# Kernel optimization log

Hardware: AMD Instinct MI355X
Metric: run time of the kernel (lower is better)

The kernel has to match this reference:

```python
import jax, jax.numpy as jnp
import numpy as np

N_GRAPHS = 8
NODES_PER_G = 1024
EDGES_PER_G = 2048
N = N_GRAPHS * NODES_PER_G          # 8192 nodes
E = N_GRAPHS * EDGES_PER_G          # 16384 edges
IN_DIM, EDGE_DIM, HID, OUT_DIM, T = 10, 9, 64, 3, 5
EPS = 1e-6


def _lin(key, fan_in, fan_out):
    kw, kb = jax.random.split(key)
    s = 1.0 / np.sqrt(fan_in)
    return (jax.random.uniform(kw, (fan_in, fan_out), jnp.float32, -s, s),
            jax.random.uniform(kb, (fan_out,), jnp.float32, -s, s))


def setup_inputs() -> dict:
    key = jax.random.key(0)
    ks = jax.random.split(key, 32)
    x = jax.random.normal(ks[0], (N, IN_DIM), jnp.float32)
    edge_attr = jax.random.normal(ks[1], (E, EDGE_DIM), jnp.float32)
    # edges stay within their own graph (block structure)
    src_l = jax.random.randint(ks[2], (E,), 0, NODES_PER_G)
    dst_l = jax.random.randint(ks[3], (E,), 0, NODES_PER_G)
    off = jnp.repeat(jnp.arange(N_GRAPHS, dtype=jnp.int64) * NODES_PER_G, EDGES_PER_G)
    edge_index = jnp.stack([src_l.astype(jnp.int64) + off, dst_l.astype(jnp.int64) + off])
    batch = jnp.repeat(jnp.arange(N_GRAPHS, dtype=jnp.int64), NODES_PER_G)

    lift_w1, lift_b1 = _lin(ks[4], IN_DIM, HID)
    lift_w2, lift_b2 = _lin(ks[5], HID, HID)
    proj_w1, proj_b1 = _lin(ks[6], HID, HID)
    proj_w2, proj_b2 = _lin(ks[7], HID, OUT_DIM)

    def stackp(fn, base):
        ws, bs = zip(*[fn(ks[base + t]) for t in range(T)])
        return jnp.stack(ws), jnp.stack(bs)

    root_w, root_b = stackp(lambda k: _lin(k, HID, HID), 8)
    k_w1, k_b1 = stackp(lambda k: _lin(k, EDGE_DIM, HID), 13)
    k_w2, k_b2 = stackp(lambda k: _lin(k, HID, HID), 18)
    k_w3, k_b3 = stackp(lambda k: _lin(k, HID, HID * HID), 23)

    return dict(x=x, edge_attr=edge_attr,
                lift_w1=lift_w1, lift_b1=lift_b1, lift_w2=lift_w2, lift_b2=lift_b2,
                root_w=root_w, root_b=root_b,
                k_w1=k_w1, k_b1=k_b1, k_w2=k_w2, k_b2=k_b2, k_w3=k_w3, k_b3=k_b3,
                proj_w1=proj_w1, proj_b1=proj_b1, proj_w2=proj_w2, proj_b2=proj_b2,
                edge_index=edge_index, batch=batch)


def reference(x, edge_attr, lift_w1, lift_b1, lift_w2, lift_b2,
              root_w, root_b, k_w1, k_b1, k_w2, k_b2, k_w3, k_b3,
              proj_w1, proj_b1, proj_w2, proj_b2, edge_index, batch):
    src, dst = edge_index[0], edge_index[1]

    # --- per-graph edge_attr standardization (scatter mean/std over each graph's edges) ---
    eb = batch[src]                                           # graph id per edge [E]
    ones_e = jnp.ones((E,), jnp.float32)
    cnt = jax.ops.segment_sum(ones_e, eb, num_segments=N_GRAPHS)          # [G]
    mean = jax.ops.segment_sum(edge_attr, eb, num_segments=N_GRAPHS) / cnt[:, None]
    msq = jax.ops.segment_sum(edge_attr * edge_attr, eb, num_segments=N_GRAPHS) / cnt[:, None]
    std = jnp.sqrt(jnp.clip(msq - mean * mean, 0.0))
    ea = (edge_attr - mean[eb]) / (std[eb] + EPS)             # [E, edge_dim]

    # --- lift MLP ---
    v = jax.nn.relu(x @ lift_w1 + lift_b1) @ lift_w2 + lift_b2  # [N, HID]

    # --- T kernel layers: v' = relu(W_root v + mean_{j->i} K(e_ij) v_j) ---
    deg = jnp.clip(jax.ops.segment_sum(ones_e, dst, num_segments=N), 1.0)  # [N]
    for t in range(T):
        h = jax.nn.relu(ea @ k_w1[t] + k_b1[t])
        h = jax.nn.relu(h @ k_w2[t] + k_b2[t])
        ker = (h @ k_w3[t] + k_b3[t]).reshape(E, HID, HID)    # per-edge 64x64 kernel
        msg = jnp.einsum('eij,ej->ei', ker, v[src])           # [E, HID]
        aggr = jax.ops.segment_sum(msg, dst, num_segments=N) / deg[:, None]
        v = jax.nn.relu(v @ root_w[t] + root_b[t] + aggr)
        # dropout (p=0.1) is identity in eval mode

    # --- project MLP ---
    return jax.nn.relu(v @ proj_w1 + proj_b1) @ proj_w2 + proj_b2  # [N, OUT_DIM]
```

## Files before the change

kernel.cpp:

```cpp
#include <hip/hip_runtime.h>

#define N_GRAPHS    8
#define EDGES_PER_G 2048
#define NN          8192
#define EE          16384
#define IN_DIM      10
#define EDGE_DIM    9
#define HID         64
#define OUT_DIM     3
#define TT          5
#define EPSN        1e-6f

typedef float f32x4 __attribute__((ext_vector_type(4)));
typedef short bf16x8s __attribute__((ext_vector_type(8)));

union BF8 { __bf16 h[8]; bf16x8s v; };

__device__ inline void gl_lds16(const unsigned short* g, unsigned short* l) {
  __builtin_amdgcn_global_load_lds(
      (const __attribute__((address_space(1))) unsigned int*)g,
      (__attribute__((address_space(3))) unsigned int*)l, 16, 0, 0);
}

__device__ inline void edgemlp16(int e0, int tid,
    const float* __restrict__ ear, const float* __restrict__ meanb,
    const float* __restrict__ invstd,
    const float* __restrict__ w1, const float* __restrict__ b1,
    const float* __restrict__ w2, const float* __restrict__ b2,
    float* smem, float* __restrict__ h2T) {
  float (*sh)[68] = (float (*)[68])smem;
  float (*st)[68] = (float (*)[68])(smem + 16 * 68);
  int g = tid >> 6, lane = tid & 63;
  int eb = e0 + g * 4;
  int gg = e0 >> 11;
  const float* mb = meanb + gg * EDGE_DIM;
  const float* is = invstd + gg * EDGE_DIM;
  float xn[4][EDGE_DIM];
#pragma unroll
  for (int k = 0; k < 4; ++k) {
    const float* er = ear + (size_t)(eb + k) * EDGE_DIM;
#pragma unroll
    for (int d = 0; d < EDGE_DIM; ++d) xn[k][d] = (er[d] - mb[d]) * is[d];
  }
  float a0 = b1[lane], a1 = a0, a2 = a0, a3 = a0;
#pragma unroll
  for (int d = 0; d < EDGE_DIM; ++d) {
    float w = w1[d * HID + lane];
    a0 += xn[0][d] * w; a1 += xn[1][d] * w;
    a2 += xn[2][d] * w; a3 += xn[3][d] * w;
  }
  sh[g * 4 + 0][lane] = fmaxf(a0, 0.f);
  sh[g * 4 + 1][lane] = fmaxf(a1, 0.f);
  sh[g * 4 + 2][lane] = fmaxf(a2, 0.f);
  sh[g * 4 + 3][lane] = fmaxf(a3, 0.f);
  __syncthreads();
  float o0 = b2[lane], o1 = o0, o2 = o0, o3 = o0;
#pragma unroll
  for (int h = 0; h < HID; ++h) {
    float w = w2[h * HID + lane];
    o0 += sh[g * 4 + 0][h] * w; o1 += sh[g * 4 + 1][h] * w;
    o2 += sh[g * 4 + 2][h] * w; o3 += sh[g * 4 + 3][h] * w;
  }
  st[g * 4 + 0][lane] = fmaxf(o0, 0.f);
  st[g * 4 + 1][lane] = fmaxf(o1, 0.f);
  st[g * 4 + 2][lane] = fmaxf(o2, 0.f);
  st[g * 4 + 3][lane] = fmaxf(o3, 0.f);
  __syncthreads();
  for (int i = tid; i < HID * 16; i += 256) {
    int c = i >> 4, eo = i & 15;
    h2T[(size_t)c * EE + e0 + eo] = st[eo][c];
  }
}

__global__ __launch_bounds__(256) void k_stats(
    const float* __restrict__ ear, float* __restrict__ meanb,
    float* __restrict__ invstd, float* __restrict__ degf) {
  __shared__ float sw[4][2 * EDGE_DIM];
  int b = blockIdx.x;
  int g = threadIdx.x >> 6, lane = threadIdx.x & 63;
  if (b < N_GRAPHS) {
    int gg = b;
    float ls[EDGE_DIM], lq[EDGE_DIM];
#pragma unroll
    for (int d = 0; d < EDGE_DIM; ++d) { ls[d] = 0.f; lq[d] = 0.f; }
    for (int e = threadIdx.x; e < EDGES_PER_G; e += blockDim.x) {
      const float* row = ear + (size_t)(gg * EDGES_PER_G + e) * EDGE_DIM;
#pragma unroll
      for (int d = 0; d < EDGE_DIM; ++d) { float xv = row[d]; ls[d] += xv; lq[d] += xv * xv; }
    }
#pragma unroll
    for (int d = 0; d < EDGE_DIM; ++d) {
#pragma unroll
      for (int off = 32; off > 0; off >>= 1) {
        ls[d] += __shfl_down(ls[d], off);
        lq[d] += __shfl_down(lq[d], off);
      }
    }
    if (lane == 0) {
#pragma unroll
      for (int d = 0; d < EDGE_DIM; ++d) {
        sw[g][d] = ls[d];
        sw[g][EDGE_DIM + d] = lq[d];
      }
    }
    __syncthreads();
    if (threadIdx.x < EDGE_DIM) {
      int d = threadIdx.x;
      float s0 = sw[0][d] + sw[1][d] + sw[2][d] + sw[3][d];
      float q0 = sw[0][EDGE_DIM + d] + sw[1][EDGE_DIM + d] +
                 sw[2][EDGE_DIM + d] + sw[3][EDGE_DIM + d];
      float m  = s0 * (1.0f / EDGES_PER_G);
      float mq = q0 * (1.0f / EDGES_PER_G);
      float var = fmaxf(mq - m * m, 0.f);
      meanb[gg * EDGE_DIM + d]  = m;
      invstd[gg * EDGE_DIM + d] = 1.f / (sqrtf(var) + EPSN);
    }
  } else {
    int idx = (b - N_GRAPHS) * 256 + threadIdx.x;
    ((float4*)degf)[idx] = make_float4(0.f, 0.f, 0.f, 0.f);
  }
}

#define PRE_EM0   (EE / 16)
#define PRE_LIFT  (NN / 4)
#define PRE_BPREP 1024
#define PRE_DEG   (EE / 256)
__global__ __launch_bounds__(256) void k_pre(
    const float* __restrict__ x,
    const float* __restrict__ lw1, const float* __restrict__ lb1,
    const float* __restrict__ lw2, const float* __restrict__ lb2,
    float* __restrict__ v,
    const float* __restrict__ kw3, const float* __restrict__ kb3,
    unsigned short* __restrict__ Bbf,
    const int* __restrict__ dst, float* __restrict__ degf,
    const float* __restrict__ ear, const float* __restrict__ meanb,
    const float* __restrict__ invstd,
    const float* __restrict__ w1, const float* __restrict__ b1,
    const float* __restrict__ w2, const float* __restrict__ b2,
    float* __restrict__ h2T0) {
  __shared__ float smem[2 * 16 * 68];
  int b = blockIdx.x;
  int g = threadIdx.x >> 6, lane = threadIdx.x & 63;
  if (b < PRE_EM0) {
    edgemlp16(b * 16, threadIdx.x, ear, meanb, invstd, w1, b1, w2, b2,
              smem, h2T0);
  } else if (b < PRE_EM0 + PRE_LIFT) {
    float (*sh)[HID] = (float (*)[HID])smem;
    int n = (b - PRE_EM0) * 4 + g;
    const float* xr = x + n * IN_DIM;
    float a = lb1[lane];
#pragma unroll
    for (int d = 0; d < IN_DIM; ++d) a += xr[d] * lw1[d * HID + lane];
    sh[g][lane] = fmaxf(a, 0.f);
    __syncthreads();
    float o = lb2[lane];
#pragma unroll
    for (int h = 0; h < HID; ++h) o += sh[g][h] * lw2[h * HID + lane];
    v[n * HID + lane] = o;
  } else if (b < PRE_EM0 + PRE_LIFT + PRE_BPREP) {
    const int total = TT * 65 * 4096;
    for (int i = (b - (PRE_EM0 + PRE_LIFT)) * 256 + (int)threadIdx.x; i < total;
         i += PRE_BPREP * 256) {
      int xx   = i & 4095;
      int call = i >> 12;
      int t = call / 65;
      int c = call - t * 65;
      int sn = xx >> 9;
      int s  = sn >> 2, nt = sn & 3;
      int l9 = xx & 511;
      int ln = l9 >> 3, jj = l9 & 7;
      int nn15 = ln & 15, qq = ln >> 4;
      int x_in = (nt * 16 + nn15) * 64 + s * 32 + qq * 8 + jj;
      float val = (c < 64) ? kw3[(size_t)(t * 64 + c) * 4096 + x_in]
                           : kb3[(size_t)t * 4096 + x_in];
      union { __bf16 h; unsigned short s16; } u;
      u.h = (__bf16)val;
      Bbf[i] = u.s16;
    }
  } else {
    int e = (b - (PRE_EM0 + PRE_LIFT + PRE_BPREP)) * 256 + threadIdx.x;
    atomicAdd(&degf[dst[e]], 1.f);
  }
}

__global__ __launch_bounds__(256) void k_csr1(const float* __restrict__ degf,
    int* __restrict__ rowptr, int* __restrict__ cur) {
  __shared__ int ps[256];
  int tid = threadIdx.x;
  int base = tid * 32;
  int loc[32];
  int s = 0;
#pragma unroll
  for (int k = 0; k < 32; ++k) { loc[k] = s; s += (int)degf[base + k]; }
  ps[tid] = s;
  __syncthreads();
  if (tid == 0) {
    int a = 0;
    for (int i = 0; i < 256; ++i) { int t = ps[i]; ps[i] = a; a += t; }
    rowptr[NN] = a;
  }
  __syncthreads();
  int off = ps[tid];
#pragma unroll
  for (int k = 0; k < 32; ++k) {
    rowptr[base + k] = off + loc[k];
    cur[base + k]    = off + loc[k];
  }
}

__global__ __launch_bounds__(256) void k_csr2(const int* __restrict__ dst,
    int* __restrict__ cur, int* __restrict__ ecsr) {
  int e = blockIdx.x * 256 + threadIdx.x;
  int d = dst[e];
  int pos = atomicAdd(&cur[d], 1);
  ecsr[pos] = e;
}

__global__ __launch_bounds__(256) void k_msg(const float* __restrict__ v,
    const float* __restrict__ h2T_r, const unsigned short* __restrict__ Bt,
    const int* __restrict__ src,
    float* __restrict__ msgbuf, int nEm,
    const float* __restrict__ ear, const float* __restrict__ meanb,
    const float* __restrict__ invstd,
    const float* __restrict__ w1, const float* __restrict__ b1,
    const float* __restrict__ w2, const float* __restrict__ b2,
    float* __restrict__ h2T_w) {
  __shared__ unsigned short bstage[3][4096];
  int b = blockIdx.x;
  if (b < 1024) {
    int kchunk = b & 3;
    int ebb    = (b >> 2) * 64;
    int w    = threadIdx.x >> 6;
    int lane = threadIdx.x & 63;
    int n15  = lane & 15;
    int q    = lane >> 4;
    int ebase = ebb + w * 16;

    bf16x8s ubf[2];
    {
      int e = ebase + n15;
      const float4* vr = (const float4*)(v + (size_t)src[e] * HID);
      int f0 = q * 2;
#pragma unroll
      for (int s = 0; s < 2; ++s) {
        float4 pa = vr[s * 8 + f0], pb = vr[s * 8 + f0 + 1];
        BF8 u;
        u.h[0] = (__bf16)pa.x; u.h[1] = (__bf16)pa.y;
        u.h[2] = (__bf16)pa.z; u.h[3] = (__bf16)pa.w;
        u.h[4] = (__bf16)pb.x; u.h[5] = (__bf16)pb.y;
        u.h[6] = (__bf16)pb.z; u.h[7] = (__bf16)pb.w;
        ubf[s] = u.v;
      }
    }

    f32x4 acc[4];
#pragma unroll
    for (int nt = 0; nt < 4; ++nt) acc[nt] = (f32x4)0.0f;

    int c0 = kchunk * 16;
    const float* hq = h2T_r + (size_t)c0 * EE + ebase + q * 4;
    const int NCC = (kchunk == 3) ? 17 : 16;

    auto stage = [&](int cc) {
      const unsigned short* gt = (cc < 16)
          ? Bt + (size_t)(c0 + cc) * 4096
          : Bt + (size_t)64 * 4096;
      const unsigned short* gsrc = gt + w * 1024 + lane * 8;
      unsigned short* ldst = &bstage[cc % 3][w * 1024];
      gl_lds16(gsrc, ldst);
      gl_lds16(gsrc + 512, ldst + 512);
    };

    stage(0);
    stage(1);

    for (int cc = 0; cc < NCC; ++cc) {
      asm volatile("s_waitcnt vmcnt(2)" ::: "memory");
      __builtin_amdgcn_s_barrier();
      float4 h4;
      if (cc < 16) h4 = *(const float4*)(hq + (size_t)cc * EE);
      __builtin_amdgcn_sched_barrier(0);
      if (cc + 2 < NCC) stage(cc + 2);
      __builtin_amdgcn_sched_barrier(0);

      const unsigned short* Bs = &bstage[cc % 3][lane * 8];
      bf16x8s bfr[2][4];
#pragma unroll
      for (int s = 0; s < 2; ++s)
#pragma unroll
        for (int nt = 0; nt < 4; ++nt)
          bfr[s][nt] = *(const bf16x8s*)(Bs + (s * 4 + nt) * 512);
      if (cc < 16) {
        f32x4 tmp[4];
#pragma unroll
        for (int nt = 0; nt < 4; ++nt) {
          f32x4 t0 = __builtin_amdgcn_mfma_f32_16x16x32_bf16(
              ubf[0], bfr[0][nt], (f32x4)0.0f, 0, 0, 0);
          tmp[nt] = __builtin_amdgcn_mfma_f32_16x16x32_bf16(
              ubf[1], bfr[1][nt], t0, 0, 0, 0);
        }
#pragma unroll
        for (int nt = 0; nt < 4; ++nt) {
          acc[nt][0] += h4.x * tmp[nt][0];
          acc[nt][1] += h4.y * tmp[nt][1];
          acc[nt][2] += h4.z * tmp[nt][2];
          acc[nt][3] += h4.w * tmp[nt][3];
        }
      } else {
#pragma unroll
        for (int s = 0; s < 2; ++s)
#pragma unroll
          for (int nt = 0; nt < 4; ++nt)
            acc[nt] = __builtin_amdgcn_mfma_f32_16x16x32_bf16(
                ubf[s], bfr[s][nt], acc[nt], 0, 0, 0);
      }
    }

    float* mb = msgbuf + (size_t)kchunk * EE * HID;
#pragma unroll
    for (int r = 0; r < 4; ++r) {
      int e = ebase + q * 4 + r;
#pragma unroll
      for (int nt = 0; nt < 4; ++nt)
        mb[(size_t)e * HID + nt * 16 + n15] = acc[nt][r];
    }
  } else if (b < 1024 + nEm) {
    edgemlp16((b - 1024) * 16, threadIdx.x, ear, meanb, invstd,
              w1, b1, w2, b2, (float*)bstage, h2T_w);
  }
}

__global__ __launch_bounds__(256) void k_upd(
    float* __restrict__ v, const float* __restrict__ rw, const float* __restrict__ rb,
    const float* __restrict__ msgbuf, const float* __restrict__ degf,
    const int* __restrict__ rowptr, const int* __restrict__ ecsr) {
  __shared__ float sh[4][HID];
  int g = threadIdx.x >> 6, lane = threadIdx.x & 63;
  int n = blockIdx.x * 4 + g;
  int idx = n * HID + lane;
  sh[g][lane] = v[idx];
  __syncthreads();
  int r0 = rowptr[n], r1 = rowptr[n + 1];
  float s = 0.f;
  for (int j = r0; j < r1; ++j) {
    int e = ecsr[j];
    s += msgbuf[(size_t)e * HID + lane]
       + msgbuf[((size_t)EE + e) * HID + lane]
       + msgbuf[((size_t)2 * EE + e) * HID + lane]
       + msgbuf[((size_t)3 * EE + e) * HID + lane];
  }
  float inv = 1.f / fmaxf(degf[n], 1.f);
  float o = rb[lane] + s * inv;
#pragma unroll
  for (int h = 0; h < HID; ++h) o += sh[g][h] * rw[h * HID + lane];
  v[idx] = fmaxf(o, 0.f);
}

__global__ __launch_bounds__(256) void k_upd_proj(
    const float* __restrict__ v, const float* __restrict__ rw,
    const float* __restrict__ rb,
    const float* __restrict__ msgbuf, const float* __restrict__ degf,
    const int* __restrict__ rowptr, const int* __restrict__ ecsr,
    const float* __restrict__ pw1, const float* __restrict__ pb1,
    const float* __restrict__ pw2, const float* __restrict__ pb2,
    float* __restrict__ out) {
  __shared__ float sh[4][HID];
  int g = threadIdx.x >> 6, lane = threadIdx.x & 63;
  int n = blockIdx.x * 4 + g;
  int idx = n * HID + lane;
  sh[g][lane] = v[idx];
  __syncthreads();
  int r0 = rowptr[n], r1 = rowptr[n + 1];
  float s = 0.f;
  for (int j = r0; j < r1; ++j) {
    int e = ecsr[j];
    s += msgbuf[(size_t)e * HID + lane]
       + msgbuf[((size_t)EE + e) * HID + lane]
       + msgbuf[((size_t)2 * EE + e) * HID + lane]
       + msgbuf[((size_t)3 * EE + e) * HID + lane];
  }
  float inv = 1.f / fmaxf(degf[n], 1.f);
  float o = rb[lane] + s * inv;
#pragma unroll
  for (int h = 0; h < HID; ++h) o += sh[g][h] * rw[h * HID + lane];
  float vn = fmaxf(o, 0.f);
  __syncthreads();
  sh[g][lane] = vn;
  __syncthreads();
  float a = pb1[lane];
#pragma unroll
  for (int h = 0; h < HID; ++h) a += sh[g][h] * pw1[h * HID + lane];
  float h1 = fmaxf(a, 0.f);
  __syncthreads();
  sh[g][lane] = h1;
  __syncthreads();
  if (lane < OUT_DIM) {
    float oo = pb2[lane];
#pragma unroll
    for (int h = 0; h < HID; ++h) oo += sh[g][h] * pw2[h * OUT_DIM + lane];
    out[n * OUT_DIM + lane] = oo;
  }
}

extern "C" void kernel_launch(void* const* d_in, const int* in_sizes, int n_in,
                              void* d_out, int out_size, void* d_ws, size_t ws_size,
                              hipStream_t stream) {
  const float* x        = (const float*)d_in[0];
  const float* ear      = (const float*)d_in[1];
  const float* lift_w1  = (const float*)d_in[2];
  const float* lift_b1  = (const float*)d_in[3];
  const float* lift_w2  = (const float*)d_in[4];
  const float* lift_b2  = (const float*)d_in[5];
  const float* root_w   = (const float*)d_in[6];
  const float* root_b   = (const float*)d_in[7];
  const float* kw1      = (const float*)d_in[8];
  const float* kb1      = (const float*)d_in[9];
  const float* kw2      = (const float*)d_in[10];
  const float* kb2      = (const float*)d_in[11];
  const float* kw3      = (const float*)d_in[12];
  const float* kb3      = (const float*)d_in[13];
  const float* pw1      = (const float*)d_in[14];
  const float* pb1      = (const float*)d_in[15];
  const float* pw2      = (const float*)d_in[16];
  const float* pb2      = (const float*)d_in[17];
  const int* edge_index = (const int*)d_in[18];
  const int* src = edge_index;
  const int* dst = edge_index + EE;
  float* out = (float*)d_out;

  float* ws     = (float*)d_ws;
  float* msgbuf = ws;
  float* degf   = msgbuf + (size_t)4 * EE * HID;
  float* h2Ta   = degf + NN;
  float* h2Tb   = h2Ta + (size_t)HID * EE;
  float* vbuf   = h2Tb + (size_t)HID * EE;
  float* meanb  = vbuf + NN * HID;
  float* invstd = meanb + 72;
  unsigned short* Bbf = (unsigned short*)(invstd + 72);
  int* rowptr = (int*)(Bbf + (size_t)TT * 65 * 4096);
  int* cur    = rowptr + NN + 1;
  int* ecsr   = cur + NN;

  k_stats<<<2 * N_GRAPHS, 256, 0, stream>>>(ear, meanb, invstd, degf);

  const int PRE_BLOCKS = PRE_EM0 + PRE_LIFT + PRE_BPREP + PRE_DEG;
  k_pre<<<PRE_BLOCKS, 256, 0, stream>>>(
      x, lift_w1, lift_b1, lift_w2, lift_b2, vbuf, kw3, kb3, Bbf,
      dst, degf, ear, meanb, invstd,
      kw1, kb1, kw2, kb2, h2Ta);

  k_csr1<<<1, 256, 0, stream>>>(degf, rowptr, cur);
  k_csr2<<<EE / 256, 256, 0, stream>>>(dst, cur, ecsr);

  for (int t = 0; t < TT; ++t) {
    const float* hr = (t & 1) ? h2Tb : h2Ta;
    float*       hw = (t & 1) ? h2Ta : h2Tb;
    int nEm = (t < TT - 1) ? EE / 16 : 0;
    int tt  = (t < TT - 1) ? t + 1 : t;
    k_msg<<<1024 + nEm, 256, 0, stream>>>(
        vbuf, hr, Bbf + (size_t)t * 65 * 4096, src, msgbuf, nEm,
        ear, meanb, invstd,
        kw1 + (size_t)tt * EDGE_DIM * HID, kb1 + (size_t)tt * HID,
        kw2 + (size_t)tt * HID * HID, kb2 + (size_t)tt * HID, hw);
    if (t < TT - 1) {
      k_upd<<<NN / 4, 256, 0, stream>>>(
          vbuf, root_w + (size_t)t * HID * HID, root_b + (size_t)t * HID,
          msgbuf, degf, rowptr, ecsr);
    } else {
      k_upd_proj<<<NN / 4, 256, 0, stream>>>(
          vbuf, root_w + (size_t)t * HID * HID, root_b + (size_t)t * HID,
          msgbuf, degf, rowptr, ecsr, pw1, pb1, pw2, pb2, out);
    }
  }
}
```

Measured before the change: 325.1 us.

## Tile two edge M-tiles per wave and split K into eight chunks

Each message-block now handles 128 edges (32 per wave, two MFMA M-tiles) over an 8-column K chunk instead of 64 edges over 16 columns. Every staged B tile in LDS is reused by twice as many MFMAs, which halves B staging traffic per edge. The cost is eight partial message buffers instead of four, so the workspace doubles and the update kernels do eight gathered reads per edge. Accumulator register count also doubles, which may lower occupancy.

Result: slower. 473.5 us (+45.7%).

```diff
diff --git a/kernel.cpp b/kernel.cpp
--- a/kernel.cpp
+++ b/kernel.cpp
@@ -228,17 +228,18 @@
   __shared__ unsigned short bstage[3][4096];
   int b = blockIdx.x;
   if (b < 1024) {
-    int kchunk = b & 3;
-    int ebb    = (b >> 2) * 64;
+    int kchunk = b & 7;
+    int ebb    = (b >> 3) * 128;
     int w    = threadIdx.x >> 6;
     int lane = threadIdx.x & 63;
     int n15  = lane & 15;
     int q    = lane >> 4;
-    int ebase = ebb + w * 16;
-
-    bf16x8s ubf[2];
-    {
-      int e = ebase + n15;
+    int ebase = ebb + w * 32;
+
+    bf16x8s ubf[2][2];
+#pragma unroll
+    for (int mt = 0; mt < 2; ++mt) {
+      int e = ebase + mt * 16 + n15;
       const float4* vr = (const float4*)(v + (size_t)src[e] * HID);
       int f0 = q * 2;
 #pragma unroll
@@ -249,20 +250,22 @@
         u.h[2] = (__bf16)pa.z; u.h[3] = (__bf16)pa.w;
         u.h[4] = (__bf16)pb.x; u.h[5] = (__bf16)pb.y;
         u.h[6] = (__bf16)pb.z; u.h[7] = (__bf16)pb.w;
-        ubf[s] = u.v;
-      }
-    }
-
-    f32x4 acc[4];
-#pragma unroll
-    for (int nt = 0; nt < 4; ++nt) acc[nt] = (f32x4)0.0f;
-
-    int c0 = kchunk * 16;
+        ubf[mt][s] = u.v;
+      }
+    }
+
+    f32x4 acc[2][4];
+#pragma unroll
+    for (int mt = 0; mt < 2; ++mt)
+#pragma unroll
+      for (int nt = 0; nt < 4; ++nt) acc[mt][nt] = (f32x4)0.0f;
+
+    int c0 = kchunk * 8;
     const float* hq = h2T_r + (size_t)c0 * EE + ebase + q * 4;
-    const int NCC = (kchunk == 3) ? 17 : 16;
+    const int NCC = (kchunk == 7) ? 9 : 8;
 
     auto stage = [&](int cc) {
-      const unsigned short* gt = (cc < 16)
+      const unsigned short* gt = (cc < 8)
           ? Bt + (size_t)(c0 + cc) * 4096
           : Bt + (size_t)64 * 4096;
       const unsigned short* gsrc = gt + w * 1024 + lane * 8;
@@ -277,8 +280,11 @@
     for (int cc = 0; cc < NCC; ++cc) {
       asm volatile("s_waitcnt vmcnt(2)" ::: "memory");
       __builtin_amdgcn_s_barrier();
-      float4 h4;
-      if (cc < 16) h4 = *(const float4*)(hq + (size_t)cc * EE);
+      float4 h4[2];
+      if (cc < 8) {
+        h4[0] = *(const float4*)(hq + (size_t)cc * EE);
+        h4[1] = *(const float4*)(hq + (size_t)cc * EE + 16);
+      }
       __builtin_amdgcn_sched_barrier(0);
       if (cc + 2 < NCC) stage(cc + 2);
       __builtin_amdgcn_sched_barrier(0);
@@ -290,39 +296,48 @@
 #pragma unroll
         for (int nt = 0; nt < 4; ++nt)
           bfr[s][nt] = *(const bf16x8s*)(Bs + (s * 4 + nt) * 512);
-      if (cc < 16) {
-        f32x4 tmp[4];
-#pragma unroll
-        for (int nt = 0; nt < 4; ++nt) {
-          f32x4 t0 = __builtin_amdgcn_mfma_f32_16x16x32_bf16(
-              ubf[0], bfr[0][nt], (f32x4)0.0f, 0, 0, 0);
-          tmp[nt] = __builtin_amdgcn_mfma_f32_16x16x32_bf16(
-              ubf[1], bfr[1][nt], t0, 0, 0, 0);
-        }
-#pragma unroll
-        for (int nt = 0; nt < 4; ++nt) {
-          acc[nt][0] += h4.x * tmp[nt][0];
-          acc[nt][1] += h4.y * tmp[nt][1];
-          acc[nt][2] += h4.z * tmp[nt][2];
-          acc[nt][3] += h4.w * tmp[nt][3];
+      if (cc < 8) {
+#pragma unroll
+        for (int mt = 0; mt < 2; ++mt) {
+          f32x4 tmp[4];
+#pragma unroll
+          for (int nt = 0; nt < 4; ++nt) {
+            f32x4 t0 = __builtin_amdgcn_mfma_f32_16x16x32_bf16(
+                ubf[mt][0], bfr[0][nt], (f32x4)0.0f, 0, 0, 0);
+            tmp[nt] = __builtin_amdgcn_mfma_f32_16x16x32_bf16(
+                ubf[mt][1], bfr[1][nt], t0, 0, 0, 0);
+          }
+          float4 hh = h4[mt];
+#pragma unroll
+          for (int nt = 0; nt < 4; ++nt) {
+            acc[mt][nt][0] += hh.x * tmp[nt][0];
+            acc[mt][nt][1] += hh.y * tmp[nt][1];
+            acc[mt][nt][2] += hh.z * tmp[nt][2];
+            acc[mt][nt][3] += hh.w * tmp[nt][3];
+          }
         }
       } else {
 #pragma unroll
         for (int s = 0; s < 2; ++s)
 #pragma unroll
-          for (int nt = 0; nt < 4; ++nt)
-            acc[nt] = __builtin_amdgcn_mfma_f32_16x16x32_bf16(
-                ubf[s], bfr[s][nt], acc[nt], 0, 0, 0);
+          for (int mt = 0; mt < 2; ++mt)
+#pragma unroll
+            for (int nt = 0; nt < 4; ++nt)
+              acc[mt][nt] = __builtin_amdgcn_mfma_f32_16x16x32_bf16(
+                  ubf[mt][s], bfr[s][nt], acc[mt][nt], 0, 0, 0);
       }
     }
 
     float* mb = msgbuf + (size_t)kchunk * EE * HID;
 #pragma unroll
-    for (int r = 0; r < 4; ++r) {
-      int e = ebase + q * 4 + r;
-#pragma unroll
-      for (int nt = 0; nt < 4; ++nt)
-        mb[(size_t)e * HID + nt * 16 + n15] = acc[nt][r];
+    for (int mt = 0; mt < 2; ++mt) {
+#pragma unroll
+      for (int r = 0; r < 4; ++r) {
+        int e = ebase + mt * 16 + q * 4 + r;
+#pragma unroll
+        for (int nt = 0; nt < 4; ++nt)
+          mb[(size_t)e * HID + nt * 16 + n15] = acc[mt][nt][r];
+      }
     }
   } else if (b < 1024 + nEm) {
     edgemlp16((b - 1024) * 16, threadIdx.x, ear, meanb, invstd,
@@ -343,11 +358,10 @@
   int r0 = rowptr[n], r1 = rowptr[n + 1];
   float s = 0.f;
   for (int j = r0; j < r1; ++j) {
-    int e = ecsr[j];
-    s += msgbuf[(size_t)e * HID + lane]
-       + msgbuf[((size_t)EE + e) * HID + lane]
-       + msgbuf[((size_t)2 * EE + e) * HID + lane]
-       + msgbuf[((size_t)3 * EE + e) * HID + lane];
+    size_t e = (size_t)ecsr[j];
+#pragma unroll
+    for (int k = 0; k < 8; ++k)
+      s += msgbuf[((size_t)k * EE + e) * HID + lane];
   }
   float inv = 1.f / fmaxf(degf[n], 1.f);
   float o = rb[lane] + s * inv;
@@ -373,11 +387,10 @@
   int r0 = rowptr[n], r1 = rowptr[n + 1];
   float s = 0.f;
   for (int j = r0; j < r1; ++j) {
-    int e = ecsr[j];
-    s += msgbuf[(size_t)e * HID + lane]
-       + msgbuf[((size_t)EE + e) * HID + lane]
-       + msgbuf[((size_t)2 * EE + e) * HID + lane]
-       + msgbuf[((size_t)3 * EE + e) * HID + lane];
+    size_t e = (size_t)ecsr[j];
+#pragma unroll
+    for (int k = 0; k < 8; ++k)
+      s += msgbuf[((size_t)k * EE + e) * HID + lane];
   }
   float inv = 1.f / fmaxf(degf[n], 1.f);
   float o = rb[lane] + s * inv;
@@ -430,7 +443,7 @@
 
   float* ws     = (float*)d_ws;
   float* msgbuf = ws;
-  float* degf   = msgbuf + (size_t)4 * EE * HID;
+  float* degf   = msgbuf + (size_t)8 * EE * HID;
   float* h2Ta   = degf + NN;
   float* h2Tb   = h2Ta + (size_t)HID * EE;
   float* vbuf   = h2Tb + (size_t)HID * EE;
```
